# Kernel optimization log

Hardware: AMD Instinct MI355X
Metric: run time of the kernel (lower is better)

## Reference

```python
import jax, jax.numpy as jnp
import numpy as np


def setup_inputs() -> dict:
    key = jax.random.key(0)
    k1, k2 = jax.random.split(key)
    q_embed = jax.random.normal(k1, (1000, 1024), dtype=jnp.float32)      # (V, D)
    conv_feat = jax.random.normal(k2, (64, 1024, 800), dtype=jnp.float32)  # (B, D, T)
    return {"q_embed": q_embed, "conv_feat": conv_feat}


def reference(q_embed, conv_feat):
    # sim_scores: (B, V, T) = q_embed (V, D) @ conv_feat (B, D, T), no scaling
    sim_scores = jnp.einsum('vd,bdt->bvt', q_embed, conv_feat)
    attention_weights = jax.nn.softmax(sim_scores, axis=2)  # over T
    # context: (B, V, D) = weights (B, V, T) @ conv_feat^T (B, T, D)
    context_vector = jnp.einsum('bvt,bdt->bvd', attention_weights, conv_feat)
    return (context_vector, attention_weights)
```

## Files before the change

### kernel.cpp

```cpp
#include <hip/hip_runtime.h>
#include <hip/hip_bf16.h>

typedef short bf16x8 __attribute__((ext_vector_type(8)));
typedef float f32x4 __attribute__((ext_vector_type(4)));

#define NV 1000
#define ND 1024
#define NT 800
#define NB 64

__device__ inline unsigned short f32_bf16(float f) {
    unsigned u = __builtin_bit_cast(unsigned, f);
    return (unsigned short)((u + 0x7FFFu + ((u >> 16) & 1u)) >> 16);
}
__device__ inline void split_bf16(float f, unsigned short& h, unsigned short& l) {
    unsigned u = __builtin_bit_cast(unsigned, f);
    unsigned hb = (u + 0x7FFFu + ((u >> 16) & 1u)) >> 16;
    h = (unsigned short)hb;
    float hf = __builtin_bit_cast(float, hb << 16);
    float lf = f - hf;
    unsigned ul = __builtin_bit_cast(unsigned, lf);
    l = (unsigned short)((ul + 0x7FFFu + ((ul >> 16) & 1u)) >> 16);
}

__device__ inline void gload16(const void* g, void* l) {
    __builtin_amdgcn_global_load_lds(
        (const __attribute__((address_space(1))) unsigned int*)g,
        (__attribute__((address_space(3))) unsigned int*)l, 16, 0, 0);
}

__global__ __launch_bounds__(256) void prep_q(const float* __restrict__ Q,
                                              unsigned short* __restrict__ Qh,
                                              unsigned short* __restrict__ Ql) {
    int idx = blockIdx.x * 256 + threadIdx.x;
    int row = idx >> 8;
    int c4 = (idx & 255) << 2;
    float4 f = make_float4(0.f, 0.f, 0.f, 0.f);
    if (row < NV) f = *(const float4*)(Q + (size_t)row * ND + c4);
    unsigned short h0,h1,h2,h3,l0,l1,l2,l3;
    split_bf16(f.x,h0,l0); split_bf16(f.y,h1,l1);
    split_bf16(f.z,h2,l2); split_bf16(f.w,h3,l3);
    *(ushort4*)(Qh + (size_t)row * ND + c4) = make_ushort4(h0,h1,h2,h3);
    *(ushort4*)(Ql + (size_t)row * ND + c4) = make_ushort4(l0,l1,l2,l3);
}

__global__ __launch_bounds__(256) void prep_c(const float* __restrict__ C,
                                              unsigned short* __restrict__ Cth,
                                              unsigned short* __restrict__ Ctl,
                                              unsigned short* __restrict__ Cbf,
                                              int writeCbf) {
    const int dt = blockIdx.x;
    const int tt = blockIdx.y;
    const int b  = blockIdx.z;
    const int tid = threadIdx.x;
    __shared__ float T[64][33];
    const float* Cb = C + (size_t)b * ND * NT;
    const int d0 = dt * 64, t0 = tt * 32;
#pragma unroll
    for (int r = 0; r < 2; ++r) {
        int idx = r * 256 + tid;
        int row = idx >> 3;
        int c4 = (idx & 7) << 2;
        float4 f = *(const float4*)(Cb + (size_t)(d0 + row) * NT + t0 + c4);
        T[row][c4 + 0] = f.x; T[row][c4 + 1] = f.y;
        T[row][c4 + 2] = f.z; T[row][c4 + 3] = f.w;
        if (writeCbf) {
            *(ushort4*)(Cbf + ((size_t)b * ND + d0 + row) * NT + t0 + c4) =
                make_ushort4(f32_bf16(f.x), f32_bf16(f.y), f32_bf16(f.z), f32_bf16(f.w));
        }
    }
    __syncthreads();
#pragma unroll
    for (int r = 0; r < 2; ++r) {
        int idx = r * 256 + tid;
        int trow = idx >> 4;
        int dc = (idx & 15) << 2;
        unsigned short h[4], l[4];
#pragma unroll
        for (int j = 0; j < 4; ++j) split_bf16(T[dc + j][trow], h[j], l[j]);
        size_t o = ((size_t)b * NT + t0 + trow) * ND + d0 + dc;
        *(ushort4*)(Cth + o) = make_ushort4(h[0],h[1],h[2],h[3]);
        *(ushort4*)(Ctl + o) = make_ushort4(l[0],l[1],l[2],l[3]);
    }
}

__global__ __launch_bounds__(256) void gemm1_kernel(const unsigned short* __restrict__ Qh,
                                                    const unsigned short* __restrict__ Ql,
                                                    const unsigned short* __restrict__ Cth,
                                                    const unsigned short* __restrict__ Ctl,
                                                    float* __restrict__ S) {
    const int h = blockIdx.x;
    const int L = (h & 7) * 320 + (h >> 3);
    const int bm = L & 7;
    const int rest = L >> 3;
    const int bn = rest % 5;
    const int b  = rest / 5;

    const int tid = threadIdx.x;
    const int lane = tid & 63;
    const int w = tid >> 6;
    const int wr = w >> 1, wc = w & 1;

    __shared__ unsigned short Ah[128 * 32];
    __shared__ unsigned short Al[128 * 32];
    __shared__ unsigned short Bh[160 * 32];
    __shared__ unsigned short Bl[160 * 32];

    const int v0 = bm * 128, t0 = bn * 160;
    const unsigned short* Agh = Qh + (size_t)v0 * ND;
    const unsigned short* Agl = Ql + (size_t)v0 * ND;
    const unsigned short* Bgh = Cth + ((size_t)b * NT + t0) * ND;
    const unsigned short* Bgl = Ctl + ((size_t)b * NT + t0) * ND;

    f32x4 acc[4][5];
#pragma unroll
    for (int i = 0; i < 4; ++i)
#pragma unroll
        for (int j = 0; j < 5; ++j) acc[i][j] = (f32x4){0.f, 0.f, 0.f, 0.f};

    const int srow = lane >> 2;
    const int sslot = lane & 3;
    const int swz = (sslot ^ (srow & 3) ^ ((srow >> 2) & 3)) << 3;

    for (int k0 = 0; k0 < ND; k0 += 32) {
        for (int i = w; i < 8; i += 4) {
            int row = i * 16 + srow;
            gload16(Agh + (size_t)row * ND + swz + k0, Ah + i * 512);
            gload16(Agl + (size_t)row * ND + swz + k0, Al + i * 512);
        }
        for (int i = w; i < 10; i += 4) {
            int row = i * 16 + srow;
            gload16(Bgh + (size_t)row * ND + swz + k0, Bh + i * 512);
            gload16(Bgl + (size_t)row * ND + swz + k0, Bl + i * 512);
        }
        __syncthreads();

        const int g = lane >> 4, rl = lane & 15;
        const int sx = (g ^ (rl & 3) ^ ((rl >> 2) & 3)) << 4;
        bf16x8 ah[4], al[4], bh[5], bl[5];
#pragma unroll
        for (int mf = 0; mf < 4; ++mf) {
            int off = (wr * 64 + mf * 16 + rl) * 64 + sx;
            ah[mf] = *(const bf16x8*)((const char*)Ah + off);
            al[mf] = *(const bf16x8*)((const char*)Al + off);
        }
#pragma unroll
        for (int nf = 0; nf < 5; ++nf) {
            int off = (wc * 80 + nf * 16 + rl) * 64 + sx;
            bh[nf] = *(const bf16x8*)((const char*)Bh + off);
            bl[nf] = *(const bf16x8*)((const char*)Bl + off);
        }
#pragma unroll
        for (int mf = 0; mf < 4; ++mf)
#pragma unroll
            for (int nf = 0; nf < 5; ++nf) {
                acc[mf][nf] = __builtin_amdgcn_mfma_f32_16x16x32_bf16(ah[mf], bh[nf], acc[mf][nf], 0, 0, 0);
                acc[mf][nf] = __builtin_amdgcn_mfma_f32_16x16x32_bf16(ah[mf], bl[nf], acc[mf][nf], 0, 0, 0);
                acc[mf][nf] = __builtin_amdgcn_mfma_f32_16x16x32_bf16(al[mf], bh[nf], acc[mf][nf], 0, 0, 0);
            }
        __syncthreads();
    }

    float* Sb = S + (size_t)b * NV * NT;
    const int g = lane >> 4, rl = lane & 15;
#pragma unroll
    for (int mf = 0; mf < 4; ++mf) {
#pragma unroll
        for (int nf = 0; nf < 5; ++nf) {
#pragma unroll
            for (int r = 0; r < 4; ++r) {
                int v = v0 + wr * 64 + mf * 16 + g * 4 + r;
                int t = t0 + wc * 80 + nf * 16 + rl;
                if (v < NV) Sb[(size_t)v * NT + t] = acc[mf][nf][r];
            }
        }
    }
}

__global__ __launch_bounds__(256) void softmax_kernel(float* __restrict__ S,
                                                      unsigned short* __restrict__ Wbf,
                                                      int writeWbf) {
    const int row = blockIdx.x * 4 + (threadIdx.x >> 6);
    const int lane = threadIdx.x & 63;
    float4* p4 = (float4*)(S + (size_t)row * NT);
    unsigned short* pw = Wbf + (size_t)row * NT;
    float4 v[4];
    float m = -INFINITY;
#pragma unroll
    for (int i = 0; i < 4; ++i) {
        int idx = i * 64 + lane;
        if (idx < 200) {
            v[i] = p4[idx];
            m = fmaxf(m, fmaxf(fmaxf(v[i].x, v[i].y), fmaxf(v[i].z, v[i].w)));
        }
    }
#pragma unroll
    for (int off = 32; off; off >>= 1) m = fmaxf(m, __shfl_xor(m, off));
    float s = 0.f;
#pragma unroll
    for (int i = 0; i < 4; ++i) {
        int idx = i * 64 + lane;
        if (idx < 200) {
            v[i].x = __expf(v[i].x - m); v[i].y = __expf(v[i].y - m);
            v[i].z = __expf(v[i].z - m); v[i].w = __expf(v[i].w - m);
            s += (v[i].x + v[i].y) + (v[i].z + v[i].w);
        }
    }
#pragma unroll
    for (int off = 32; off; off >>= 1) s += __shfl_xor(s, off);
    const float inv = 1.0f / s;
#pragma unroll
    for (int i = 0; i < 4; ++i) {
        int idx = i * 64 + lane;
        if (idx < 200) {
            float4 o = make_float4(v[i].x * inv, v[i].y * inv, v[i].z * inv, v[i].w * inv);
            p4[idx] = o;
            if (writeWbf)
                *(ushort4*)(pw + idx * 4) =
                    make_ushort4(f32_bf16(o.x), f32_bf16(o.y), f32_bf16(o.z), f32_bf16(o.w));
        }
    }
}

__global__ __launch_bounds__(512) void gemm2_fast(const unsigned short* __restrict__ Wbf,
                                                  const unsigned short* __restrict__ Cbf,
                                                  float* __restrict__ O) {
    const int h = blockIdx.x;
    const int L = (h & 7) * 128 + (h >> 3);
    const int b  = L >> 4;
    const int bm = (L >> 2) & 3;
    const int bn = L & 3;
    const int tid = threadIdx.x;
    const int lane = tid & 63;
    const int w = tid >> 6;
    const int wr = w >> 2, wc = w & 3;

    __shared__ unsigned short lds[4 * 16384];

    const int v0 = bm * 256, d0 = bn * 256;
    const unsigned short* Ag = Wbf + (size_t)b * NV * NT;
    const unsigned short* Bg = Cbf + ((size_t)b * ND + d0) * NT;

    f32x4 acc[8][4];
#pragma unroll
    for (int i = 0; i < 8; ++i)
#pragma unroll
        for (int j = 0; j < 4; ++j) acc[i][j] = (f32x4){0.f, 0.f, 0.f, 0.f};

    const int srow = lane >> 2;
    const int sslot = lane & 3;
    const int swz = (sslot ^ (srow & 3) ^ ((srow >> 2) & 3)) << 3;
    const int g = lane >> 4, rl = lane & 15;
    const int sx = (g ^ (rl & 3) ^ ((rl >> 2) & 3)) << 4;

#define G2_STAGE(K0, BUF)                                                     \
    {                                                                         \
        unsigned short* Lb = lds + (BUF) * 16384;                             \
        _Pragma("unroll")                                                     \
        for (int i = w; i < 16; i += 8) {                                     \
            int row = i * 16 + srow;                                          \
            int vrow = v0 + row; if (vrow > NV - 1) vrow = NV - 1;            \
            gload16(Ag + (size_t)vrow * NT + swz + (K0), Lb + i * 512);       \
            gload16(Bg + (size_t)row * NT + swz + (K0), Lb + 8192 + i * 512); \
        }                                                                     \
    }

#define G2_COMPUTE(BUF)                                                       \
    {                                                                         \
        const char* Lb = (const char*)(lds + (BUF) * 16384);                  \
        bf16x8 bq[4];                                                         \
        _Pragma("unroll")                                                     \
        for (int nf = 0; nf < 4; ++nf)                                        \
            bq[nf] = *(const bf16x8*)(Lb + 16384 + (wc * 64 + nf * 16 + rl) * 64 + sx); \
        _Pragma("unroll")                                                     \
        for (int p = 0; p < 4; ++p) {                                         \
            bf16x8 a0 = *(const bf16x8*)(Lb + (wr * 128 + (2 * p) * 16 + rl) * 64 + sx);     \
            bf16x8 a1 = *(const bf16x8*)(Lb + (wr * 128 + (2 * p + 1) * 16 + rl) * 64 + sx); \
            __builtin_amdgcn_s_setprio(1);                                    \
            _Pragma("unroll")                                                 \
            for (int nf = 0; nf < 4; ++nf)                                    \
                acc[2 * p][nf] = __builtin_amdgcn_mfma_f32_16x16x32_bf16(a0, bq[nf], acc[2 * p][nf], 0, 0, 0); \
            _Pragma("unroll")                                                 \
            for (int nf = 0; nf < 4; ++nf)                                    \
                acc[2 * p + 1][nf] = __builtin_amdgcn_mfma_f32_16x16x32_bf16(a1, bq[nf], acc[2 * p + 1][nf], 0, 0, 0); \
            __builtin_amdgcn_s_setprio(0);                                    \
        }                                                                     \
    }

    G2_STAGE(0, 0);
    G2_STAGE(32, 1);
    G2_STAGE(64, 2);
#pragma unroll 1
    for (int t = 0; t < 22; ++t) {
        G2_STAGE((t + 3) * 32, (t + 3) & 3);
        asm volatile("s_waitcnt vmcnt(12)\n\ts_barrier" ::: "memory");
        G2_COMPUTE(t & 3);
        asm volatile("s_waitcnt lgkmcnt(0)\n\ts_barrier" ::: "memory");
    }
    asm volatile("s_waitcnt vmcnt(8)\n\ts_barrier" ::: "memory");
    G2_COMPUTE(22 & 3);
    asm volatile("s_waitcnt lgkmcnt(0)\n\ts_barrier" ::: "memory");
    asm volatile("s_waitcnt vmcnt(4)\n\ts_barrier" ::: "memory");
    G2_COMPUTE(23 & 3);
    asm volatile("s_waitcnt lgkmcnt(0)\n\ts_barrier" ::: "memory");
    asm volatile("s_waitcnt vmcnt(0)\n\ts_barrier" ::: "memory");
    G2_COMPUTE(24 & 3);

    float* Ob = O + (size_t)b * NV * ND;
#pragma unroll
    for (int mf = 0; mf < 8; ++mf) {
#pragma unroll
        for (int nf = 0; nf < 4; ++nf) {
#pragma unroll
            for (int r = 0; r < 4; ++r) {
                int v = v0 + wr * 128 + mf * 16 + g * 4 + r;
                int d = d0 + wc * 64 + nf * 16 + rl;
                if (v < NV) Ob[(size_t)v * ND + d] = acc[mf][nf][r];
            }
        }
    }
#undef G2_STAGE
#undef G2_COMPUTE
}

__global__ __launch_bounds__(256) void gemm2_mid(const unsigned short* __restrict__ Wbf,
                                                 const float* __restrict__ C,
                                                 float* __restrict__ O) {
    const int h = blockIdx.x;
    const int L = (h & 7) * 512 + (h >> 3);
    const int bm = L & 7;
    const int bn = (L >> 3) & 7;
    const int b  = L >> 6;
    const int tid = threadIdx.x;
    const int lane = tid & 63;
    const int w = tid >> 6;
    const int wr = w >> 1, wc = w & 1;

    __shared__ unsigned short As[128 * 32];
    __shared__ unsigned short Bs[128][40];

    const int v0 = bm * 128, d0 = bn * 128;
    const unsigned short* Ag = Wbf + (size_t)b * NV * NT;
    const float* Cb = C + (size_t)b * ND * NT;

    f32x4 acc[4][4];
#pragma unroll
    for (int i = 0; i < 4; ++i)
#pragma unroll
        for (int j = 0; j < 4; ++j) acc[i][j] = (f32x4){0.f, 0.f, 0.f, 0.f};

    const int srow = lane >> 2;
    const int sslot = lane & 3;

    for (int k0 = 0; k0 < NT; k0 += 32) {
        for (int i = w; i < 8; i += 4) {
            int row = i * 16 + srow;
            int c = ((sslot ^ (row & 3)) << 3) + k0;
            int vrow = v0 + row; if (vrow > NV - 1) vrow = NV - 1;
            gload16(Ag + (size_t)vrow * NT + c, As + i * 512);
        }
#pragma unroll
        for (int r = 0; r < 4; ++r) {
            int idx = r * 256 + tid;
            int row = idx >> 3;
            int kq  = (idx & 7) << 2;
            const float4 f = *(const float4*)(Cb + (size_t)(d0 + row) * NT + k0 + kq);
            *(ushort4*)&Bs[row][kq] = make_ushort4(f32_bf16(f.x), f32_bf16(f.y), f32_bf16(f.z), f32_bf16(f.w));
        }
        __syncthreads();

        const int g = lane >> 4, rl = lane & 15;
        const int sx = (g ^ (rl & 3)) << 4;
        const int kk = g << 3;
        bf16x8 a[4], bfr[4];
#pragma unroll
        for (int mf = 0; mf < 4; ++mf) {
            int off = (wr * 64 + mf * 16 + rl) * 64 + sx;
            a[mf] = *(const bf16x8*)((const char*)As + off);
        }
#pragma unroll
        for (int nf = 0; nf < 4; ++nf) {
            int row = wc * 64 + nf * 16 + rl;
            bfr[nf] = *(const bf16x8*)&Bs[row][kk];
        }
#pragma unroll
        for (int mf = 0; mf < 4; ++mf)
#pragma unroll
            for (int nf = 0; nf < 4; ++nf)
                acc[mf][nf] = __builtin_amdgcn_mfma_f32_16x16x32_bf16(a[mf], bfr[nf], acc[mf][nf], 0, 0, 0);
        __syncthreads();
    }

    float* Ob = O + (size_t)b * NV * ND;
    const int g = lane >> 4, rl = lane & 15;
#pragma unroll
    for (int mf = 0; mf < 4; ++mf) {
#pragma unroll
        for (int nf = 0; nf < 4; ++nf) {
#pragma unroll
            for (int r = 0; r < 4; ++r) {
                int v = v0 + wr * 64 + mf * 16 + g * 4 + r;
                int d = d0 + wc * 64 + nf * 16 + rl;
                if (v < NV) Ob[(size_t)v * ND + d] = acc[mf][nf][r];
            }
        }
    }
}

__global__ __launch_bounds__(256) void gemm2_slow(const float* __restrict__ W,
                                                  const float* __restrict__ C,
                                                  float* __restrict__ O) {
    const int h = blockIdx.x;
    const int L = (h & 7) * 512 + (h >> 3);
    const int bm = L & 7;
    const int bn = (L >> 3) & 7;
    const int b  = L >> 6;
    const int tid = threadIdx.x;
    const int lane = tid & 63;
    const int wid = tid >> 6;
    const int wr = wid >> 1;
    const int wc = wid & 1;

    __shared__ unsigned short As[128][40];
    __shared__ unsigned short Bs[128][40];

    const float* Wb = W + (size_t)b * NV * NT;
    const float* Cb = C + (size_t)b * ND * NT;
    const int v0 = bm * 128;
    const int d0 = bn * 128;

    f32x4 acc[4][4];
#pragma unroll
    for (int i = 0; i < 4; ++i)
#pragma unroll
        for (int j = 0; j < 4; ++j) acc[i][j] = (f32x4){0.f, 0.f, 0.f, 0.f};

    for (int k0 = 0; k0 < NT; k0 += 32) {
#pragma unroll
        for (int r = 0; r < 4; ++r) {
            int idx = r * 256 + tid;
            int row = idx >> 3;
            int kq  = (idx & 7) << 2;
            int v = v0 + row; if (v > NV - 1) v = NV - 1;
            const float4 f = *(const float4*)(Wb + (size_t)v * NT + k0 + kq);
            *(ushort4*)&As[row][kq] = make_ushort4(f32_bf16(f.x), f32_bf16(f.y), f32_bf16(f.z), f32_bf16(f.w));
        }
#pragma unroll
        for (int r = 0; r < 4; ++r) {
            int idx = r * 256 + tid;
            int row = idx >> 3;
            int kq  = (idx & 7) << 2;
            const float4 f = *(const float4*)(Cb + (size_t)(d0 + row) * NT + k0 + kq);
            *(ushort4*)&Bs[row][kq] = make_ushort4(f32_bf16(f.x), f32_bf16(f.y), f32_bf16(f.z), f32_bf16(f.w));
        }
        __syncthreads();

        bf16x8 a[4], bfr[4];
        const int kk = (lane >> 4) << 3;
#pragma unroll
        for (int mf = 0; mf < 4; ++mf) {
            int row = wr * 64 + mf * 16 + (lane & 15);
            a[mf] = *(const bf16x8*)&As[row][kk];
        }
#pragma unroll
        for (int nf = 0; nf < 4; ++nf) {
            int row = wc * 64 + nf * 16 + (lane & 15);
            bfr[nf] = *(const bf16x8*)&Bs[row][kk];
        }
#pragma unroll
        for (int mf = 0; mf < 4; ++mf)
#pragma unroll
            for (int nf = 0; nf < 4; ++nf)
                acc[mf][nf] = __builtin_amdgcn_mfma_f32_16x16x32_bf16(a[mf], bfr[nf], acc[mf][nf], 0, 0, 0);
        __syncthreads();
    }

    float* Ob = O + (size_t)b * NV * ND;
#pragma unroll
    for (int mf = 0; mf < 4; ++mf) {
#pragma unroll
        for (int nf = 0; nf < 4; ++nf) {
#pragma unroll
            for (int r = 0; r < 4; ++r) {
                int v = v0 + wr * 64 + mf * 16 + (lane >> 4) * 4 + r;
                int d = d0 + wc * 64 + nf * 16 + (lane & 15);
                if (v < NV) Ob[(size_t)v * ND + d] = acc[mf][nf][r];
            }
        }
    }
}

extern "C" void kernel_launch(void* const* d_in, const int* in_sizes, int n_in,
                              void* d_out, int out_size, void* d_ws, size_t ws_size,
                              hipStream_t stream) {
    const float* Q = (const float*)d_in[0];
    const float* C = (const float*)d_in[1];
    float* ctx = (float*)d_out;
    float* wts = ctx + (size_t)NB * NV * ND;

    unsigned short* Cth = (unsigned short*)ctx;
    unsigned short* Ctl = Cth + (size_t)NB * NT * ND;
    unsigned short* Qh  = Ctl + (size_t)NB * NT * ND;
    unsigned short* Ql  = Qh + (size_t)1024 * ND;

    const size_t WbfBytes = (size_t)NB * NV * NT * 2;
    const size_t CbfBytes = (size_t)NB * ND * NT * 2;
    unsigned short* Wbf = (unsigned short*)d_ws;
    unsigned short* Cbf = (unsigned short*)((char*)d_ws + WbfBytes);
    const int wsFast = ws_size >= WbfBytes + CbfBytes;
    const int wsMid  = ws_size >= WbfBytes;

    prep_q<<<dim3(1024), 256, 0, stream>>>(Q, Qh, Ql);
    prep_c<<<dim3(16, 25, NB), 256, 0, stream>>>(C, Cth, Ctl, Cbf, wsFast);
    gemm1_kernel<<<dim3(2560), 256, 0, stream>>>(Qh, Ql, Cth, Ctl, wts);
    softmax_kernel<<<dim3(16000), 256, 0, stream>>>(wts, Wbf, wsMid);
    if (wsFast)      gemm2_fast<<<dim3(1024), 512, 0, stream>>>(Wbf, Cbf, ctx);
    else if (wsMid)  gemm2_mid<<<dim3(4096), 256, 0, stream>>>(Wbf, C, ctx);
    else             gemm2_slow<<<dim3(4096), 256, 0, stream>>>(wts, C, ctx);
}
```

Before: 671.0 us.

## Enlarge gemm1 tile to 256x160 and shrink gemm2 pipeline to double buffering

gemm1 now gives each block a 256-row by 160-column output tile with four waves stacked along V, each holding 4x10 accumulators. This halves the block count and increases operand reuse from LDS. gemm2_fast drops its 4-stage LDS ring for a simple 2-buffer ping-pong, loads all A fragments up front and removes the setprio hints. The intent is to cut LDS footprint and raise occupancy, at the cost of a shallower prefetch that may expose memory latency, and higher register pressure in gemm1.

Result: slower. 766.8 us (+14.3%).

```diff
diff --git a/kernel.cpp b/kernel.cpp
--- a/kernel.cpp
+++ b/kernel.cpp
@@ -90,40 +90,41 @@
                                                     const unsigned short* __restrict__ Ctl,
                                                     float* __restrict__ S) {
     const int h = blockIdx.x;
-    const int L = (h & 7) * 320 + (h >> 3);
-    const int bm = L & 7;
-    const int rest = L >> 3;
+    const int L = (h & 7) * 160 + (h >> 3);
+    const int bm = L & 3;
+    const int rest = L >> 2;
     const int bn = rest % 5;
     const int b  = rest / 5;
 
     const int tid = threadIdx.x;
     const int lane = tid & 63;
     const int w = tid >> 6;
-    const int wr = w >> 1, wc = w & 1;
-
-    __shared__ unsigned short Ah[128 * 32];
-    __shared__ unsigned short Al[128 * 32];
+
+    __shared__ unsigned short Ah[256 * 32];
+    __shared__ unsigned short Al[256 * 32];
     __shared__ unsigned short Bh[160 * 32];
     __shared__ unsigned short Bl[160 * 32];
 
-    const int v0 = bm * 128, t0 = bn * 160;
+    const int v0 = bm * 256, t0 = bn * 160;
     const unsigned short* Agh = Qh + (size_t)v0 * ND;
     const unsigned short* Agl = Ql + (size_t)v0 * ND;
     const unsigned short* Bgh = Cth + ((size_t)b * NT + t0) * ND;
     const unsigned short* Bgl = Ctl + ((size_t)b * NT + t0) * ND;
 
-    f32x4 acc[4][5];
+    f32x4 acc[4][10];
 #pragma unroll
     for (int i = 0; i < 4; ++i)
 #pragma unroll
-        for (int j = 0; j < 5; ++j) acc[i][j] = (f32x4){0.f, 0.f, 0.f, 0.f};
+        for (int j = 0; j < 10; ++j) acc[i][j] = (f32x4){0.f, 0.f, 0.f, 0.f};
 
     const int srow = lane >> 2;
     const int sslot = lane & 3;
     const int swz = (sslot ^ (srow & 3) ^ ((srow >> 2) & 3)) << 3;
+    const int g = lane >> 4, rl = lane & 15;
+    const int sx = (g ^ (rl & 3) ^ ((rl >> 2) & 3)) << 4;
 
     for (int k0 = 0; k0 < ND; k0 += 32) {
-        for (int i = w; i < 8; i += 4) {
+        for (int i = w; i < 16; i += 4) {
             int row = i * 16 + srow;
             gload16(Agh + (size_t)row * ND + swz + k0, Ah + i * 512);
             gload16(Agl + (size_t)row * ND + swz + k0, Al + i * 512);
@@ -135,25 +136,23 @@
         }
         __syncthreads();
 
-        const int g = lane >> 4, rl = lane & 15;
-        const int sx = (g ^ (rl & 3) ^ ((rl >> 2) & 3)) << 4;
-        bf16x8 ah[4], al[4], bh[5], bl[5];
+        bf16x8 ah[4], al[4], bh[10], bl[10];
 #pragma unroll
         for (int mf = 0; mf < 4; ++mf) {
-            int off = (wr * 64 + mf * 16 + rl) * 64 + sx;
+            int off = (w * 64 + mf * 16 + rl) * 64 + sx;
             ah[mf] = *(const bf16x8*)((const char*)Ah + off);
             al[mf] = *(const bf16x8*)((const char*)Al + off);
         }
 #pragma unroll
-        for (int nf = 0; nf < 5; ++nf) {
-            int off = (wc * 80 + nf * 16 + rl) * 64 + sx;
+        for (int nf = 0; nf < 10; ++nf) {
+            int off = (nf * 16 + rl) * 64 + sx;
             bh[nf] = *(const bf16x8*)((const char*)Bh + off);
             bl[nf] = *(const bf16x8*)((const char*)Bl + off);
         }
 #pragma unroll
         for (int mf = 0; mf < 4; ++mf)
 #pragma unroll
-            for (int nf = 0; nf < 5; ++nf) {
+            for (int nf = 0; nf < 10; ++nf) {
                 acc[mf][nf] = __builtin_amdgcn_mfma_f32_16x16x32_bf16(ah[mf], bh[nf], acc[mf][nf], 0, 0, 0);
                 acc[mf][nf] = __builtin_amdgcn_mfma_f32_16x16x32_bf16(ah[mf], bl[nf], acc[mf][nf], 0, 0, 0);
                 acc[mf][nf] = __builtin_amdgcn_mfma_f32_16x16x32_bf16(al[mf], bh[nf], acc[mf][nf], 0, 0, 0);
@@ -162,15 +161,14 @@
     }
 
     float* Sb = S + (size_t)b * NV * NT;
-    const int g = lane >> 4, rl = lane & 15;
 #pragma unroll
     for (int mf = 0; mf < 4; ++mf) {
 #pragma unroll
-        for (int nf = 0; nf < 5; ++nf) {
+        for (int nf = 0; nf < 10; ++nf) {
 #pragma unroll
             for (int r = 0; r < 4; ++r) {
-                int v = v0 + wr * 64 + mf * 16 + g * 4 + r;
-                int t = t0 + wc * 80 + nf * 16 + rl;
+                int v = v0 + w * 64 + mf * 16 + g * 4 + r;
+                int t = t0 + nf * 16 + rl;
                 if (v < NV) Sb[(size_t)v * NT + t] = acc[mf][nf][r];
             }
         }
@@ -235,7 +233,7 @@
     const int w = tid >> 6;
     const int wr = w >> 2, wc = w & 3;
 
-    __shared__ unsigned short lds[4 * 16384];
+    __shared__ unsigned short lds[2 * 16384];
 
     const int v0 = bm * 256, d0 = bn * 256;
     const unsigned short* Ag = Wbf + (size_t)b * NV * NT;
@@ -268,43 +266,36 @@
 #define G2_COMPUTE(BUF)                                                       \
     {                                                                         \
         const char* Lb = (const char*)(lds + (BUF) * 16384);                  \
-        bf16x8 bq[4];                                                         \
+        bf16x8 a[8], bq[4];                                                   \
         _Pragma("unroll")                                                     \
-        for (int nf = 0; nf < 4; ++nf)                                        \
-            bq[nf] = *(const bf16x8*)(Lb + 16384 + (wc * 64 + nf * 16 + rl) * 64 + sx); \
+        for (int mf = 0; mf < 8; ++mf) {                                      \
+            int off = (wr * 128 + mf * 16 + rl) * 64 + sx;                    \
+            a[mf] = *(const bf16x8*)(Lb + off);                               \
+        }                                                                     \
         _Pragma("unroll")                                                     \
-        for (int p = 0; p < 4; ++p) {                                         \
-            bf16x8 a0 = *(const bf16x8*)(Lb + (wr * 128 + (2 * p) * 16 + rl) * 64 + sx);     \
-            bf16x8 a1 = *(const bf16x8*)(Lb + (wr * 128 + (2 * p + 1) * 16 + rl) * 64 + sx); \
-            __builtin_amdgcn_s_setprio(1);                                    \
+        for (int nf = 0; nf < 4; ++nf) {                                      \
+            int off = (wc * 64 + nf * 16 + rl) * 64 + sx;                     \
+            bq[nf] = *(const bf16x8*)(Lb + 16384 + off);                      \
+        }                                                                     \
+        _Pragma("unroll")                                                     \
+        for (int mf = 0; mf < 8; ++mf)                                        \
             _Pragma("unroll")                                                 \
             for (int nf = 0; nf < 4; ++nf)                                    \
-                acc[2 * p][nf] = __builtin_amdgcn_mfma_f32_16x16x32_bf16(a0, bq[nf], acc[2 * p][nf], 0, 0, 0); \
-            _Pragma("unroll")                                                 \
-            for (int nf = 0; nf < 4; ++nf)                                    \
-                acc[2 * p + 1][nf] = __builtin_amdgcn_mfma_f32_16x16x32_bf16(a1, bq[nf], acc[2 * p + 1][nf], 0, 0, 0); \
-            __builtin_amdgcn_s_setprio(0);                                    \
-        }                                                                     \
+                acc[mf][nf] = __builtin_amdgcn_mfma_f32_16x16x32_bf16(a[mf], bq[nf], acc[mf][nf], 0, 0, 0); \
     }
 
     G2_STAGE(0, 0);
-    G2_STAGE(32, 1);
-    G2_STAGE(64, 2);
+    int cur = 0;
 #pragma unroll 1
-    for (int t = 0; t < 22; ++t) {
-        G2_STAGE((t + 3) * 32, (t + 3) & 3);
-        asm volatile("s_waitcnt vmcnt(12)\n\ts_barrier" ::: "memory");
-        G2_COMPUTE(t & 3);
+    for (int t = 0; t < 24; ++t) {
+        G2_STAGE((t + 1) * 32, cur ^ 1);
+        asm volatile("s_waitcnt vmcnt(4)\n\ts_barrier" ::: "memory");
+        G2_COMPUTE(cur);
         asm volatile("s_waitcnt lgkmcnt(0)\n\ts_barrier" ::: "memory");
-    }
-    asm volatile("s_waitcnt vmcnt(8)\n\ts_barrier" ::: "memory");
-    G2_COMPUTE(22 & 3);
-    asm volatile("s_waitcnt lgkmcnt(0)\n\ts_barrier" ::: "memory");
-    asm volatile("s_waitcnt vmcnt(4)\n\ts_barrier" ::: "memory");
-    G2_COMPUTE(23 & 3);
-    asm volatile("s_waitcnt lgkmcnt(0)\n\ts_barrier" ::: "memory");
+        cur ^= 1;
+    }
     asm volatile("s_waitcnt vmcnt(0)\n\ts_barrier" ::: "memory");
-    G2_COMPUTE(24 & 3);
+    G2_COMPUTE(cur);
 
     float* Ob = O + (size_t)b * NV * ND;
 #pragma unroll
@@ -512,7 +503,7 @@
 
     prep_q<<<dim3(1024), 256, 0, stream>>>(Q, Qh, Ql);
     prep_c<<<dim3(16, 25, NB), 256, 0, stream>>>(C, Cth, Ctl, Cbf, wsFast);
-    gemm1_kernel<<<dim3(2560), 256, 0, stream>>>(Qh, Ql, Cth, Ctl, wts);
+    gemm1_kernel<<<dim3(1280), 256, 0, stream>>>(Qh, Ql, Cth, Ctl, wts);
     softmax_kernel<<<dim3(16000), 256, 0, stream>>>(wts, Wbf, wsMid);
     if (wsFast)      gemm2_fast<<<dim3(1024), 512, 0, stream>>>(Wbf, Cbf, ctx);
     else if (wsMid)  gemm2_mid<<<dim3(4096), 256, 0, stream>>>(Wbf, C, ctx);
```
